# Optimization experiments

Measured on AMD Instinct MI355X. Metric: run time of the kernel, lower is better.

Reference implementation:

```python
import jax, jax.numpy as jnp
import numpy as np

H, W = 256, 832
B = 2
SEARCH_W, SEARCH_H = 7, 3
SPARSITY_RAD = 2
SENSE_RANGE = 10
PIX_W = 20.0          # pixel_distance_weight
ALPHA_W = 0.7         # alpha_distance_weight
MULLINE_W = 15.0      # pixel_mulline_distance_weight
ALPHA_PAD = 0.6       # alpha_padding
INF = 1e9


def _sorted_offsets(span_x, span_y):
    xs, ys = np.meshgrid(span_x, span_y)
    xs = xs.flatten(); ys = ys.flatten()
    order = np.argsort(xs ** 2 + ys ** 2, kind='stable')
    return xs[order].astype(np.int32), ys[order].astype(np.int32)


def setup_inputs() -> dict:
    key = jax.random.key(0)
    k1, k2 = jax.random.split(key)
    src = (jax.random.uniform(k1, (B, 1, H, W)) < 0.02).astype(jnp.float32)
    dst = (jax.random.uniform(k2, (B, 1, H, W)) < 0.02).astype(jnp.float32)
    xx, yy = _sorted_offsets(np.arange(-SEARCH_W, SEARCH_W + 1), np.arange(-SEARCH_H, SEARCH_H + 1))
    sxs, sys_ = np.meshgrid(np.arange(-SPARSITY_RAD, SPARSITY_RAD + 1), np.arange(-SPARSITY_RAD, SPARSITY_RAD + 1))
    sxx = sxs.flatten().astype(np.int32); syy = sys_.flatten().astype(np.int32)
    cxx, cyy = _sorted_offsets(np.arange(-SENSE_RANGE, SENSE_RANGE + 1), np.arange(-SENSE_RANGE, SENSE_RANGE + 1))
    return {"binMapsrc": src, "binMapdst": dst,
            "xx": jnp.asarray(xx), "yy": jnp.asarray(yy),
            "sxx": jnp.asarray(sxx), "syy": jnp.asarray(syy),
            "cxx": jnp.asarray(cxx), "cyy": jnp.asarray(cyy)}


def _orientation(m):
    # local edge orientation from a 3x3 box-blurred map
    b = sum(jnp.roll(jnp.roll(m, di, 0), dj, 1) for di in (-1, 0, 1) for dj in (-1, 0, 1))
    gy, gx = jnp.gradient(b)
    return jnp.arctan2(gy, gx)


def _morph_single(src, dst, xx, yy, sxx, syy, cxx, cyy):
    gy, gx = jnp.meshgrid(jnp.arange(H, dtype=jnp.int32), jnp.arange(W, dtype=jnp.int32), indexing='ij')

    def gather(offy, offx, arr, fill):
        ii = gy[None] + offy[:, None, None]          # [K,H,W]
        jj = gx[None] + offx[:, None, None]
        inb = (ii >= 0) & (ii < H) & (jj >= 0) & (jj < W)
        vals = arr[jnp.clip(ii, 0, H - 1), jnp.clip(jj, 0, W - 1)]
        return jnp.where(inb, vals, fill)

    src_e = src > 0.5
    # --- sparsify source edge points: keep min-linear-index edge in each sparsity window ---
    lin = jnp.where(src_e, (gy * W + gx).astype(jnp.float32), INF)
    keep = src_e & (lin == gather(syy, sxx, lin, INF).min(0))
    # --- windowed correspondence search with distance + orientation scoring ---
    theta_s = _orientation(src)
    theta_d = _orientation(dst)
    hit = gather(yy, xx, dst, 0.0) > 0.5             # [K,H,W]
    ang = 1.0 - jnp.cos(theta_s[None] - gather(yy, xx, theta_d, 0.0))
    dist = jnp.sqrt((xx * xx + yy * yy).astype(jnp.float32))
    score = jnp.where(hit, PIX_W * dist[:, None, None] + MULLINE_W * ALPHA_W * ang, INF)
    kbest = jnp.argmin(score, axis=0)                # [H,W]
    active = keep & (score.min(0) < 0.5 * INF)
    dispx = jnp.where(active, xx[kbest].astype(jnp.float32), 0.0)
    dispy = jnp.where(active, yy[kbest].astype(jnp.float32), 0.0)
    # --- diffuse sparse displacements over the sense window (scan keeps memory small) ---
    R = SENSE_RANGE
    pad = lambda a: jnp.pad(a, ((R, R), (R, R)))
    pdx, pdy, pm = pad(dispx), pad(dispy), pad(active.astype(jnp.float32))
    wk = jnp.exp(-jnp.sqrt((cxx * cxx + cyy * cyy).astype(jnp.float32)) / (0.5 * R))

    def body(carry, inp):
        nx, ny, den = carry
        dy_, dx_, w = inp
        sl = lambda a: jax.lax.dynamic_slice(a, (R + dy_, R + dx_), (H, W))
        return (nx + w * sl(pdx), ny + w * sl(pdy), den + w * sl(pm)), None

    zeros = jnp.zeros((H, W), jnp.float32)
    (nx, ny, den), _ = jax.lax.scan(body, (zeros, zeros, zeros), (cyy, cxx, wk))
    mdx = ALPHA_PAD * nx / (den + 1e-6)
    mdy = ALPHA_PAD * ny / (den + 1e-6)
    morphedx = gx.astype(jnp.float32) + mdx
    morphedy = gy.astype(jnp.float32) + mdy
    return jnp.stack([morphedx, morphedy], 0)        # [2,H,W]


def reference(binMapsrc, binMapdst, xx, yy, sxx, syy, cxx, cyy):
    f = lambda s, d: _morph_single(s, d, xx, yy, sxx, syy, cxx, cyy)
    return jax.vmap(f)(binMapsrc[:, 0], binMapdst[:, 0])  # [B,2,H,W]
```

## Files before the change

### kernel.cpp

```cpp
#include <hip/hip_runtime.h>
#include <math.h>

#define BB 2
#define HH 256
#define WW 832
#define HWIMG (HH * WW)

#define TS 16
#define TXN (WW / TS)
#define TYN (HH / TS)

#define KCAP 160
#define ECAP 128
#define HCAP 192

#define SRH 40
#define SRW 64
#define DRH 46
#define DRW 64

__device__ inline float theta_at(const float* __restrict__ m, int i, int j) {
    int ri[5], cj[5];
#pragma unroll
    for (int t = 0; t < 5; ++t) {
        int r = i + t - 2; r = (r < 0) ? r + HH : (r >= HH ? r - HH : r);
        int c = j + t - 2; c = (c < 0) ? c + WW : (c >= WW ? c - WW : c);
        ri[t] = r * WW; cj[t] = c;
    }
    float S[5][5];
#pragma unroll
    for (int a = 0; a < 5; ++a)
#pragma unroll
        for (int c = 0; c < 5; ++c)
            S[a][c] = m[ri[a] + cj[c]];
    float ct[5], cm[5], cb[5];
#pragma unroll
    for (int c = 0; c < 5; ++c) {
        ct[c] = S[0][c] + S[1][c] + S[2][c];
        cm[c] = S[1][c] + S[2][c] + S[3][c];
        cb[c] = S[2][c] + S[3][c] + S[4][c];
    }
    float Bm = ct[1] + ct[2] + ct[3];
    float Bp = cb[1] + cb[2] + cb[3];
    float Bl = cm[0] + cm[1] + cm[2];
    float Br = cm[2] + cm[3] + cm[4];
    float Bc = cm[1] + cm[2] + cm[3];
    float gy = (i == 0) ? (Bp - Bc) : (i == HH - 1) ? (Bc - Bm) : 0.5f * (Bp - Bm);
    float gx = (j == 0) ? (Br - Bc) : (j == WW - 1) ? (Bc - Bl) : 0.5f * (Br - Bl);
    return atan2f(gy, gx);
}

__device__ inline float theta_lds(const float* __restrict__ m, int stride,
                                  int li, int lj) {
    const float* p = m + (li - 2) * stride + (lj - 2);
    float S[5][5];
#pragma unroll
    for (int a = 0; a < 5; ++a)
#pragma unroll
        for (int c = 0; c < 5; ++c)
            S[a][c] = p[a * stride + c];
    float ct[5], cm[5], cb[5];
#pragma unroll
    for (int c = 0; c < 5; ++c) {
        ct[c] = S[0][c] + S[1][c] + S[2][c];
        cm[c] = S[1][c] + S[2][c] + S[3][c];
        cb[c] = S[2][c] + S[3][c] + S[4][c];
    }
    float Bm = ct[1] + ct[2] + ct[3];
    float Bp = cb[1] + cb[2] + cb[3];
    float Bl = cm[0] + cm[1] + cm[2];
    float Br = cm[2] + cm[3] + cm[4];
    float gy = 0.5f * (Bp - Bm);
    float gx = 0.5f * (Br - Bl);
    return atan2f(gy, gx);
}

__global__ __launch_bounds__(256) void fused_kernel(
        const float* __restrict__ src, const float* __restrict__ dst,
        const int* __restrict__ xx, const int* __restrict__ yy, int K,
        float* __restrict__ out) {
    __shared__ float slds[SRH * SRW];
    __shared__ float dlds[DRH * DRW];
    __shared__ int kox[112], koy[112];
    __shared__ float kd[112];
    __shared__ float wt[441];
    __shared__ int elist[ECAP];
    __shared__ int recs[KCAP];
    __shared__ float tss[KCAP];
    __shared__ unsigned long long best64[KCAP];
    __shared__ int hits[HCAP];
    __shared__ float4 ent[KCAP];
    __shared__ int nedge, nkeep, nhit;

    int tid = threadIdx.x;
    int lane = tid & 63;
    int wv = tid >> 6;
    int b = blockIdx.z;
    int i0 = blockIdx.y * TS;
    int j0 = blockIdx.x * TS;
    const float* sb = src + b * HWIMG;
    const float* db = dst + b * HWIMG;

    if (tid == 0) { nedge = 0; nkeep = 0; nhit = 0; }
    for (int t = tid; t < KCAP; t += 256) best64[t] = ~0ULL;

    {
        int c = j0 - 12 + lane;
        int cc = min(max(c, 0), WW - 1);
        bool cok = (c >= 0) && (c < WW);
#pragma unroll
        for (int rr = 0; rr < 10; ++rr) {
            int row = wv + 4 * rr;
            int r = i0 - 12 + row;
            int cr = min(max(r, 0), HH - 1);
            float v = sb[cr * WW + cc];
            slds[row * SRW + lane] = (cok && r >= 0 && r < HH) ? v : 0.f;
        }
    }
    {
        int c = j0 - 20 + lane;
        int cc = min(max(c, 0), WW - 1);
        bool cok = (c >= 0) && (c < WW);
#pragma unroll
        for (int rr = 0; rr < 12; ++rr) {
            int row = wv + 4 * rr;
            if (row < DRH) {
                int r = i0 - 15 + row;
                int cr = min(max(r, 0), HH - 1);
                float v = db[cr * WW + cc];
                dlds[row * DRW + lane] = (cok && r >= 0 && r < HH) ? v : 0.f;
            }
        }
    }
    for (int t = tid; t < K; t += 256) {
        int ox = xx[t], oy = yy[t];
        kox[t] = ox; koy[t] = oy;
        kd[t] = 20.0f * sqrtf((float)(ox * ox + oy * oy));
    }
    for (int t = tid; t < 21 * 32; t += 256) {
        int dy = t >> 5, dx = t & 31;
        if (dx < 21)
            wt[dy * 21 + dx] = expf(-sqrtf((float)((dx - 10) * (dx - 10) +
                                                   (dy - 10) * (dy - 10))) / 5.0f);
    }
    __syncthreads();

    for (int t = tid; t < 36 * 64; t += 256) {
        int cl = t & 63, rl = t >> 6;
        if (cl < 36 && slds[(rl + 2) * SRW + (cl + 2)] > 0.5f) {
            int p = atomicAdd(&nedge, 1);
            if (p < ECAP) elist[p] = (rl << 8) | cl;
        }
    }
    __syncthreads();

    int nE = (nedge < ECAP) ? nedge : ECAP;
    for (int t = tid; t < nE; t += 256) {
        int rl = elist[t] >> 8, cl = elist[t] & 255;
        int li = rl + 2, lj = cl + 2;
        float m = 0.f;
#pragma unroll
        for (int p = 0; p < 12; ++p) {
            int di = (p < 5) ? -2 : (p < 10 ? -1 : 0);
            int dj = (p < 5) ? (p - 2) : (p < 10 ? (p - 7) : (p - 12));
            m = fmaxf(m, slds[(li + di) * SRW + (lj + dj)]);
        }
        if (m <= 0.5f) {
            int gi = i0 - 10 + rl, gj = j0 - 10 + cl;
            bool inner = (gi >= 2) && (gi < HH - 2) && (gj >= 2) && (gj < WW - 2);
            float ts = inner ? theta_lds(slds, SRW, li, lj)
                             : theta_at(sb, gi, gj);
            int p = atomicAdd(&nkeep, 1);
            if (p < KCAP) { recs[p] = gj | (gi << 10); tss[p] = ts; }
        }
    }
    __syncthreads();

    int nk = (nkeep < KCAP) ? nkeep : KCAP;
    for (int t = tid; t < nk * 128; t += 256) {
        int w = t >> 7, k = t & 127;
        if (k < K) {
            int rec = recs[w];
            int kj = rec & 1023, ki = rec >> 10;
            int pli = ki - i0 + 15 + koy[k];
            int plj = kj - j0 + 20 + kox[k];
            if (dlds[pli * DRW + plj] > 0.5f) {
                int p = atomicAdd(&nhit, 1);
                if (p < HCAP) hits[p] = (w << 7) | k;
            }
        }
    }
    __syncthreads();

    int nh = (nhit < HCAP) ? nhit : HCAP;
    for (int t = tid; t < nh; t += 256) {
        int w = hits[t] >> 7, k = hits[t] & 127;
        int rec = recs[w];
        int kj = rec & 1023, ki = rec >> 10;
        int pi = ki + koy[k], pj = kj + kox[k];
        bool inner = (pi >= 2) && (pi < HH - 2) && (pj >= 2) && (pj < WW - 2);
        float td = inner ? theta_lds(dlds, DRW, pi - i0 + 15, pj - j0 + 20)
                         : theta_at(db, pi, pj);
        float sc = kd[k] + 10.5f * (1.0f - cosf(tss[w] - td));
        unsigned long long pk =
            ((unsigned long long)__float_as_uint(sc) << 32) | (unsigned)k;
        atomicMin(&best64[w], pk);
    }
    __syncthreads();

    for (int t = tid; t < nk; t += 256) {
        unsigned long long v = best64[t];
        if (v != ~0ULL) {
            int k = (int)(v & 0xffffffffULL);
            int rec = recs[t];
            ent[t] = make_float4((float)(rec & 1023), (float)(rec >> 10),
                                 (float)kox[k], (float)koy[k]);
        } else {
            ent[t] = make_float4(-1e4f, -1e4f, 0.f, 0.f);
        }
    }
    __syncthreads();

    int gj = j0 + (tid & 15);
    int gi = i0 + (tid >> 4);
    float nx = 0.f, ny = 0.f, de = 0.f;
    for (int w = 0; w < nk; ++w) {
        float4 E = ent[w];
        int dj = (int)E.x - gj;
        int di = (int)E.y - gi;
        if (dj >= -10 && dj <= 10 && di >= -10 && di <= 10) {
            float w_ = wt[(di + 10) * 21 + dj + 10];
            de += w_; nx += w_ * E.z; ny += w_ * E.w;
        }
    }
    float inv = 0.6f / (de + 1e-6f);
    int obase = b * 2 * HWIMG;
    out[obase + gi * WW + gj] = (float)gj + nx * inv;
    out[obase + HWIMG + gi * WW + gj] = (float)gi + ny * inv;
}

extern "C" void kernel_launch(void* const* d_in, const int* in_sizes, int n_in,
                              void* d_out, int out_size, void* d_ws, size_t ws_size,
                              hipStream_t stream) {
    const float* src = (const float*)d_in[0];
    const float* dst = (const float*)d_in[1];
    const int* xx = (const int*)d_in[2];
    const int* yy = (const int*)d_in[3];
    int K = in_sizes[2];

    float* out = (float*)d_out;
    dim3 grid(TXN, TYN, BB);
    fused_kernel<<<grid, dim3(256), 0, stream>>>(src, dst, xx, yy, K, out);
}
```

Measured before the change: 91.68 us.

## Merge edge scan with sparsity check, drop entry table and extra barriers

Replaces the two-pass edge list (atomic collect, then sparsity check) with a single pass that tests sparsity inline. Source-theta computation moves into a separate loop after the keep count is known, and the float4 entry table is removed so the final accumulation reads best64/recs/kox directly. Global loads for the halo regions are issued into registers before any LDS stores, and lanes beyond the needed columns skip loads. This removes two __syncthreads and some LDS traffic, at the cost of more indirect reads in the per-pixel accumulation loop.

```diff
diff --git a/kernel.cpp b/kernel.cpp
--- a/kernel.cpp
+++ b/kernel.cpp
@@ -11,7 +11,6 @@
 #define TYN (HH / TS)
 
 #define KCAP 160
-#define ECAP 128
 #define HCAP 192
 
 #define SRH 40
@@ -84,13 +83,11 @@
     __shared__ int kox[112], koy[112];
     __shared__ float kd[112];
     __shared__ float wt[441];
-    __shared__ int elist[ECAP];
     __shared__ int recs[KCAP];
     __shared__ float tss[KCAP];
     __shared__ unsigned long long best64[KCAP];
     __shared__ int hits[HCAP];
-    __shared__ float4 ent[KCAP];
-    __shared__ int nedge, nkeep, nhit;
+    __shared__ int nkeep, nhit;
 
     int tid = threadIdx.x;
     int lane = tid & 63;
@@ -101,41 +98,46 @@
     const float* sb = src + b * HWIMG;
     const float* db = dst + b * HWIMG;
 
-    if (tid == 0) { nedge = 0; nkeep = 0; nhit = 0; }
+    if (tid == 0) { nkeep = 0; nhit = 0; }
     for (int t = tid; t < KCAP; t += 256) best64[t] = ~0ULL;
 
+    float sv[10], dv[12];
     {
         int c = j0 - 12 + lane;
         int cc = min(max(c, 0), WW - 1);
-        bool cok = (c >= 0) && (c < WW);
+        bool cok = (c >= 0) && (c < WW) && (lane < 40);
 #pragma unroll
         for (int rr = 0; rr < 10; ++rr) {
-            int row = wv + 4 * rr;
-            int r = i0 - 12 + row;
+            int r = i0 - 12 + wv + 4 * rr;
             int cr = min(max(r, 0), HH - 1);
-            float v = sb[cr * WW + cc];
-            slds[row * SRW + lane] = (cok && r >= 0 && r < HH) ? v : 0.f;
+            float v = cok ? sb[cr * WW + cc] : 0.f;
+            sv[rr] = (r >= 0 && r < HH) ? v : 0.f;
         }
     }
     {
         int c = j0 - 20 + lane;
         int cc = min(max(c, 0), WW - 1);
-        bool cok = (c >= 0) && (c < WW);
+        bool cok = (c >= 0) && (c < WW) && (lane < 55);
 #pragma unroll
         for (int rr = 0; rr < 12; ++rr) {
             int row = wv + 4 * rr;
-            if (row < DRH) {
-                int r = i0 - 15 + row;
-                int cr = min(max(r, 0), HH - 1);
-                float v = db[cr * WW + cc];
-                dlds[row * DRW + lane] = (cok && r >= 0 && r < HH) ? v : 0.f;
-            }
-        }
-    }
-    for (int t = tid; t < K; t += 256) {
-        int ox = xx[t], oy = yy[t];
-        kox[t] = ox; koy[t] = oy;
-        kd[t] = 20.0f * sqrtf((float)(ox * ox + oy * oy));
+            int r = i0 - 15 + row;
+            int cr = min(max(r, 0), HH - 1);
+            float v = (cok && row < DRH) ? db[cr * WW + cc] : 0.f;
+            dv[rr] = (r >= 0 && r < HH) ? v : 0.f;
+        }
+    }
+#pragma unroll
+    for (int rr = 0; rr < 10; ++rr)
+        slds[(wv + 4 * rr) * SRW + lane] = sv[rr];
+#pragma unroll
+    for (int rr = 0; rr < 12; ++rr)
+        if (wv + 4 * rr < DRH) dlds[(wv + 4 * rr) * DRW + lane] = dv[rr];
+
+    if (tid < K) {
+        int ox = xx[tid], oy = yy[tid];
+        kox[tid] = ox; koy[tid] = oy;
+        kd[tid] = 20.0f * sqrtf((float)(ox * ox + oy * oy));
     }
     for (int t = tid; t < 21 * 32; t += 256) {
         int dy = t >> 5, dx = t & 31;
@@ -147,43 +149,40 @@
 
     for (int t = tid; t < 36 * 64; t += 256) {
         int cl = t & 63, rl = t >> 6;
-        if (cl < 36 && slds[(rl + 2) * SRW + (cl + 2)] > 0.5f) {
-            int p = atomicAdd(&nedge, 1);
-            if (p < ECAP) elist[p] = (rl << 8) | cl;
-        }
-    }
-    __syncthreads();
-
-    int nE = (nedge < ECAP) ? nedge : ECAP;
-    for (int t = tid; t < nE; t += 256) {
-        int rl = elist[t] >> 8, cl = elist[t] & 255;
-        int li = rl + 2, lj = cl + 2;
-        float m = 0.f;
-#pragma unroll
-        for (int p = 0; p < 12; ++p) {
-            int di = (p < 5) ? -2 : (p < 10 ? -1 : 0);
-            int dj = (p < 5) ? (p - 2) : (p < 10 ? (p - 7) : (p - 12));
-            m = fmaxf(m, slds[(li + di) * SRW + (lj + dj)]);
-        }
-        if (m <= 0.5f) {
-            int gi = i0 - 10 + rl, gj = j0 - 10 + cl;
-            bool inner = (gi >= 2) && (gi < HH - 2) && (gj >= 2) && (gj < WW - 2);
-            float ts = inner ? theta_lds(slds, SRW, li, lj)
-                             : theta_at(sb, gi, gj);
-            int p = atomicAdd(&nkeep, 1);
-            if (p < KCAP) { recs[p] = gj | (gi << 10); tss[p] = ts; }
+        if (cl < 36) {
+            int li = rl + 2, lj = cl + 2;
+            if (slds[li * SRW + lj] > 0.5f) {
+                float m = 0.f;
+#pragma unroll
+                for (int p = 0; p < 12; ++p) {
+                    int di = (p < 5) ? -2 : (p < 10 ? -1 : 0);
+                    int dj = (p < 5) ? (p - 2) : (p < 10 ? (p - 7) : (p - 12));
+                    m = fmaxf(m, slds[(li + di) * SRW + (lj + dj)]);
+                }
+                if (m <= 0.5f) {
+                    int gi = i0 - 10 + rl, gj = j0 - 10 + cl;
+                    int p = atomicAdd(&nkeep, 1);
+                    if (p < KCAP) recs[p] = gj | (gi << 10);
+                }
+            }
         }
     }
     __syncthreads();
 
     int nk = (nkeep < KCAP) ? nkeep : KCAP;
+    for (int t = tid; t < nk; t += 256) {
+        int rec = recs[t];
+        int kj = rec & 1023, ki = rec >> 10;
+        bool inner = (ki >= 2) && (ki < HH - 2) && (kj >= 2) && (kj < WW - 2);
+        tss[t] = inner ? theta_lds(slds, SRW, ki - i0 + 12, kj - j0 + 12)
+                       : theta_at(sb, ki, kj);
+    }
     for (int t = tid; t < nk * 128; t += 256) {
         int w = t >> 7, k = t & 127;
         if (k < K) {
             int rec = recs[w];
-            int kj = rec & 1023, ki = rec >> 10;
-            int pli = ki - i0 + 15 + koy[k];
-            int plj = kj - j0 + 20 + kox[k];
+            int pli = (rec >> 10) - i0 + 15 + koy[k];
+            int plj = (rec & 1023) - j0 + 20 + kox[k];
             if (dlds[pli * DRW + plj] > 0.5f) {
                 int p = atomicAdd(&nhit, 1);
                 if (p < HCAP) hits[p] = (w << 7) | k;
@@ -196,8 +195,7 @@
     for (int t = tid; t < nh; t += 256) {
         int w = hits[t] >> 7, k = hits[t] & 127;
         int rec = recs[w];
-        int kj = rec & 1023, ki = rec >> 10;
-        int pi = ki + koy[k], pj = kj + kox[k];
+        int pi = (rec >> 10) + koy[k], pj = (rec & 1023) + kox[k];
         bool inner = (pi >= 2) && (pi < HH - 2) && (pj >= 2) && (pj < WW - 2);
         float td = inner ? theta_lds(dlds, DRW, pi - i0 + 15, pj - j0 + 20)
                          : theta_at(db, pi, pj);
@@ -208,29 +206,20 @@
     }
     __syncthreads();
 
-    for (int t = tid; t < nk; t += 256) {
-        unsigned long long v = best64[t];
-        if (v != ~0ULL) {
-            int k = (int)(v & 0xffffffffULL);
-            int rec = recs[t];
-            ent[t] = make_float4((float)(rec & 1023), (float)(rec >> 10),
-                                 (float)kox[k], (float)koy[k]);
-        } else {
-            ent[t] = make_float4(-1e4f, -1e4f, 0.f, 0.f);
-        }
-    }
-    __syncthreads();
-
     int gj = j0 + (tid & 15);
     int gi = i0 + (tid >> 4);
     float nx = 0.f, ny = 0.f, de = 0.f;
     for (int w = 0; w < nk; ++w) {
-        float4 E = ent[w];
-        int dj = (int)E.x - gj;
-        int di = (int)E.y - gi;
-        if (dj >= -10 && dj <= 10 && di >= -10 && di <= 10) {
-            float w_ = wt[(di + 10) * 21 + dj + 10];
-            de += w_; nx += w_ * E.z; ny += w_ * E.w;
+        unsigned long long v = best64[w];
+        if (v != ~0ULL) {
+            int rec = recs[w];
+            int dj = (rec & 1023) - gj;
+            int di = (rec >> 10) - gi;
+            if (dj >= -10 && dj <= 10 && di >= -10 && di <= 10) {
+                int k = (int)(v & 127ULL);
+                float w_ = wt[(di + 10) * 21 + dj + 10];
+                de += w_; nx += w_ * (float)kox[k]; ny += w_ * (float)koy[k];
+            }
         }
     }
     float inv = 0.6f / (de + 1e-6f);
```

New measurement: 92.18 us. About the same (+0.5%).
